# Performance work log

Hardware: AMD Instinct MI355X
Metric: run time of the kernel (lower is better)

Reference implementation:

```python
import jax, jax.numpy as jnp
import numpy as np

NUM_HIDDEN = 256   # per-head dim == model dim in this module
NUM_HEADS = 8
SEQ_LEN = 2048
BATCH = 4
D_K = 256          # self.d_k used for the softmax scale


def setup_inputs() -> dict:
    key = jax.random.key(0)
    ks = jax.random.split(key, 12)
    H, D = NUM_HEADS, NUM_HIDDEN
    init = lambda k, shape: (jax.random.normal(k, shape, dtype=jnp.float32) * 0.02)
    return {
        "query": jax.random.normal(ks[0], (BATCH, SEQ_LEN, D), dtype=jnp.float32),
        "key": jax.random.normal(ks[1], (BATCH, SEQ_LEN, D), dtype=jnp.float32),
        "values": jax.random.normal(ks[2], (BATCH, SEQ_LEN, D), dtype=jnp.float32),
        "Wq": init(ks[3], (H * D, D)), "bq": init(ks[4], (H * D,)),
        "Wk": init(ks[5], (H * D, D)), "bk": init(ks[6], (H * D,)),
        "Wv": init(ks[7], (H * D, D)), "bv": init(ks[8], (H * D,)),
        "Wo": init(ks[9], (D, H * D)), "bo": init(ks[10], (D,)),
    }


def reference(query, key, values, Wq, bq, Wk, bk, Wv, bv, Wo, bo):
    B, S, D = query.shape
    H = Wq.shape[0] // D
    # Linear projections to [B, S, H*D], then the module's raw reshape to [B, H, S, D]
    # (note: this is a plain view, NOT the usual split-heads transpose -> faithful to source)
    q = (jnp.einsum("bsd,ed->bse", query, Wq) + bq).reshape(B, H, S, D)
    k = (jnp.einsum("bsd,ed->bse", key, Wk) + bk).reshape(B, H, S, D)
    v = (jnp.einsum("bsd,ed->bse", values, Wv) + bv).reshape(B, H, S, D)
    # scores: [B, H, S, S], scaled by sqrt(d_k); default path applies no mask
    scores = jnp.einsum("bhqd,bhkd->bhqk", q, k) / jnp.sqrt(jnp.float32(D_K))
    attn = jax.nn.softmax(scores, axis=-1)
    # dropout in eval mode: identity
    out = jnp.einsum("bhqk,bhkd->bhqd", attn, v)            # [B, H, S, D]
    out = out.transpose(0, 2, 1, 3).reshape(B, S, H * D)    # [B, S, H*D]
    return jnp.einsum("bse,de->bsd", out, Wo) + bo          # [B, S, D]
```

## Files before the change

### kernel.cpp

```cpp
#include <hip/hip_runtime.h>
#include <hip/hip_bf16.h>
#include <stdint.h>

#define B_SZ 4
#define H_N 8
#define S_LEN 2048
#define D_HEAD 256
#define HD 2048

typedef __attribute__((ext_vector_type(8))) short bf16x8;
typedef __attribute__((ext_vector_type(4))) float f32x4;
typedef __attribute__((ext_vector_type(4))) uint32_t u32x4;
typedef __hip_bfloat16 bf16;

typedef __attribute__((address_space(1))) const void glob_cv;
typedef __attribute__((address_space(3))) void lds_v;

__device__ __forceinline__ short f2bf(float f) {
  bf16 h = __float2bfloat16(f);
  return *reinterpret_cast<short*>(&h);
}

__device__ __forceinline__ uint32_t cvtpk(float lo, float hi) {
  uint32_t r;
  asm volatile("v_cvt_pk_bf16_f32 %0, %1, %2" : "=v"(r) : "v"(lo), "v"(hi));
  return r;
}

__global__ __launch_bounds__(256) void cvt_all(
    const float* __restrict__ w0, bf16* __restrict__ o0,
    const float* __restrict__ w1, bf16* __restrict__ o1,
    const float* __restrict__ w2, bf16* __restrict__ o2,
    const float* __restrict__ w3, bf16* __restrict__ o3,
    const float* __restrict__ x0, bf16* __restrict__ y0,
    const float* __restrict__ x1, bf16* __restrict__ y1,
    const float* __restrict__ x2, bf16* __restrict__ y2) {
  int bid = blockIdx.x;
  const float* src; bf16* dst; int off;
  if (bid < 1024) {
    int k = bid >> 8; off = (bid & 255) * 2048;
    src = k == 0 ? w0 : k == 1 ? w1 : k == 2 ? w2 : w3;
    dst = k == 0 ? o0 : k == 1 ? o1 : k == 2 ? o2 : o3;
  } else {
    int j = bid - 1024; int k = j >> 10; off = (j & 1023) * 2048;
    src = k == 0 ? x0 : k == 1 ? x1 : x2;
    dst = k == 0 ? y0 : k == 1 ? y1 : y2;
  }
  int i = off + threadIdx.x * 8;
  float4 a = *(const float4*)(src + i);
  float4 b = *(const float4*)(src + i + 4);
  bf16x8 o;
  o[0] = f2bf(a.x); o[1] = f2bf(a.y); o[2] = f2bf(a.z); o[3] = f2bf(a.w);
  o[4] = f2bf(b.x); o[5] = f2bf(b.y); o[6] = f2bf(b.z); o[7] = f2bf(b.w);
  *reinterpret_cast<bf16x8*>(dst + i) = o;
}

__global__ __launch_bounds__(256, 2) void proj3(
    const bf16* __restrict__ A0, const bf16* __restrict__ A1, const bf16* __restrict__ A2,
    const bf16* __restrict__ B0, const bf16* __restrict__ B1, const bf16* __restrict__ B2,
    const float* __restrict__ c0, const float* __restrict__ c1, const float* __restrict__ c2,
    bf16* __restrict__ O0, bf16* __restrict__ O1, bf16* __restrict__ O2) {
  constexpr int HALF = 2 * 128 * 128;
  __shared__ __align__(16) char lds[2 * HALF];

  int which = blockIdx.y;
  const bf16* A = which == 0 ? A0 : which == 1 ? A1 : A2;
  const bf16* Bm = which == 0 ? B0 : which == 1 ? B1 : B2;
  const float* bias = which == 0 ? c0 : which == 1 ? c1 : c2;
  bf16* OutP = which == 0 ? O0 : which == 1 ? O1 : O2;
  float scale = which == 0 ? (1.0f / 16.0f) * 1.44269504f : 1.0f;

  int tid = threadIdx.x;
  int w = tid >> 6, l = tid & 63;
  int l15 = l & 15, lg = l >> 4;
  int wr = w >> 1, wc = w & 1;

  int bid = blockIdx.x;
  int wg = (bid & 7) * 128 + (bid >> 3);
  int mt = wg >> 4, nt = wg & 15;
  int m0 = mt * 128, n0 = nt * 128;

  const size_t K2 = 512;
  char* ldsp = (char*)lds;
  const char* Abase = (const char*)A + (size_t)m0 * K2;
  const char* Bbase = (const char*)Bm + (size_t)n0 * K2;

  auto ISSUE = [&](int buf, int kt) {
    const char* As = Abase + (size_t)kt * 128;
    const char* Bs = Bbase + (size_t)kt * 128;
    char* db = ldsp + buf * HALF;
#pragma unroll
    for (int i = 0; i < 4; ++i) {
      int c = tid + i * 256, row = c >> 3;
      __builtin_amdgcn_global_load_lds((glob_cv*)(As + (size_t)row * K2 + 16 * ((c & 7) ^ (row & 7))),
                                       (lds_v*)(db + c * 16), 16, 0, 0);
    }
#pragma unroll
    for (int i = 0; i < 4; ++i) {
      int c = tid + i * 256, row = c >> 3;
      __builtin_amdgcn_global_load_lds((glob_cv*)(Bs + (size_t)row * K2 + 16 * ((c & 7) ^ (row & 7))),
                                       (lds_v*)(db + 16384 + c * 16), 16, 0, 0);
    }
  };

  f32x4 acc[4][4];
#pragma unroll
  for (int mi = 0; mi < 4; ++mi)
#pragma unroll
    for (int ni = 0; ni < 4; ++ni) acc[mi][ni] = f32x4{0.f, 0.f, 0.f, 0.f};

  ISSUE(0, 0);
  for (int kt = 0; kt < 4; ++kt) {
    int cur = kt & 1;
    if (kt < 3) {
      ISSUE(cur ^ 1, kt + 1);
      asm volatile("s_waitcnt vmcnt(8)" ::: "memory");
    } else {
      asm volatile("s_waitcnt vmcnt(0)" ::: "memory");
    }
    __builtin_amdgcn_s_barrier();
    __builtin_amdgcn_sched_barrier(0);

    const char* bufc = ldsp + cur * HALF;
#pragma unroll
    for (int kb2 = 0; kb2 < 2; ++kb2) {
      int swz = 16 * ((kb2 * 4 + lg) ^ (l15 & 7));
      bf16x8 af[4], bfr[4];
#pragma unroll
      for (int mi = 0; mi < 4; ++mi)
        af[mi] = *(const bf16x8*)(bufc + (wr * 64 + mi * 16 + l15) * 128 + swz);
#pragma unroll
      for (int ni = 0; ni < 4; ++ni)
        bfr[ni] = *(const bf16x8*)(bufc + 16384 + (wc * 64 + ni * 16 + l15) * 128 + swz);
#pragma unroll
      for (int mi = 0; mi < 4; ++mi)
#pragma unroll
        for (int ni = 0; ni < 4; ++ni)
          acc[mi][ni] = __builtin_amdgcn_mfma_f32_16x16x32_bf16(af[mi], bfr[ni], acc[mi][ni], 0, 0, 0);
    }
    __builtin_amdgcn_sched_barrier(0);
    __builtin_amdgcn_s_barrier();
  }

  if (which == 2) {
    bf16* tp = (bf16*)lds;
#pragma unroll
    for (int ni = 0; ni < 4; ++ni) {
      int colL = wc * 64 + ni * 16 + l15;
      float bv = bias[n0 + colL];
#pragma unroll
      for (int mi = 0; mi < 4; ++mi) {
        short4 pk4;
        pk4.x = f2bf(acc[mi][ni][0] + bv);
        pk4.y = f2bf(acc[mi][ni][1] + bv);
        pk4.z = f2bf(acc[mi][ni][2] + bv);
        pk4.w = f2bf(acc[mi][ni][3] + bv);
        *(short4*)(tp + colL * 136 + wr * 64 + mi * 16 + lg * 4) = pk4;
      }
    }
    __syncthreads();
    int b = m0 >> 11, h = (m0 >> 8) & 7;
    int ehi = n0 >> 8, t0 = m0 & 255;
    bf16* vb = OutP + (size_t)(b * 8 + h) * D_HEAD * S_LEN;
#pragma unroll
    for (int p = 0; p < 8; ++p) {
      int colL = p * 16 + (tid >> 4);
      int d = (n0 & 255) + colL;
      int4 v = *(const int4*)(tp + colL * 136 + (tid & 15) * 8);
      *(int4*)(vb + (size_t)d * S_LEN + ehi * 256 + t0 + (tid & 15) * 8) = v;
    }
  } else {
#pragma unroll
    for (int ni = 0; ni < 4; ++ni) {
      int col = n0 + wc * 64 + ni * 16 + l15;
      float bv = bias[col];
#pragma unroll
      for (int mi = 0; mi < 4; ++mi) {
#pragma unroll
        for (int r = 0; r < 4; ++r) {
          float v = (acc[mi][ni][r] + bv) * scale;
          int row = m0 + wr * 64 + mi * 16 + lg * 4 + r;
          int b = row >> 11;
          int h = (row >> 8) & 7;
          int d = col & 255;
          size_t off;
          if (which == 1) {
            int jj = (col >> 8) * 256 + (row & 255);
            off = (((size_t)(b * 8 + h) * S_LEN) + jj) * D_HEAD + d;
          } else {
            int sp = ((row & 255) << 3) | (col >> 8);
            off = (((size_t)(b * 8 + h) * S_LEN) + sp) * D_HEAD + d;
          }
          OutP[off] = __float2bfloat16(v);
        }
      }
    }
  }
}

__global__ __launch_bounds__(256, 2) void out_gemm(const bf16* __restrict__ A,
                                                   const bf16* __restrict__ Bm,
                                                   const float* __restrict__ bias,
                                                   float* __restrict__ Out) {
  constexpr int HALF = 2 * 64 * 128;
  __shared__ __align__(16) char lds[2 * HALF];

  int tid = threadIdx.x;
  int w = tid >> 6, l = tid & 63;
  int l15 = l & 15, lg = l >> 4;
  int wr = w >> 1, wc = w & 1;

  int bid = blockIdx.x;
  int wg = (bid & 7) * 64 + (bid >> 3);
  int mt = wg >> 2, nt = wg & 3;
  int m0 = mt * 64, n0 = nt * 64;

  const size_t K2 = 4096;
  char* ldsp = (char*)lds;
  const char* Abase = (const char*)A + (size_t)m0 * K2;
  const char* Bbase = (const char*)Bm + (size_t)n0 * K2;

  auto ISSUE = [&](int buf, int kt) {
    const char* As = Abase + (size_t)kt * 128;
    const char* Bs = Bbase + (size_t)kt * 128;
    char* db = ldsp + buf * HALF;
#pragma unroll
    for (int i = 0; i < 2; ++i) {
      int c = tid + i * 256, row = c >> 3;
      __builtin_amdgcn_global_load_lds((glob_cv*)(As + (size_t)row * K2 + 16 * ((c & 7) ^ (row & 7))),
                                       (lds_v*)(db + c * 16), 16, 0, 0);
    }
#pragma unroll
    for (int i = 0; i < 2; ++i) {
      int c = tid + i * 256, row = c >> 3;
      __builtin_amdgcn_global_load_lds((glob_cv*)(Bs + (size_t)row * K2 + 16 * ((c & 7) ^ (row & 7))),
                                       (lds_v*)(db + 8192 + c * 16), 16, 0, 0);
    }
  };

  f32x4 acc[2][2];
#pragma unroll
  for (int mi = 0; mi < 2; ++mi)
#pragma unroll
    for (int ni = 0; ni < 2; ++ni) acc[mi][ni] = f32x4{0.f, 0.f, 0.f, 0.f};

  ISSUE(0, 0);
  for (int kt = 0; kt < 32; ++kt) {
    int cur = kt & 1;
    if (kt < 31) {
      ISSUE(cur ^ 1, kt + 1);
      asm volatile("s_waitcnt vmcnt(4)" ::: "memory");
    } else {
      asm volatile("s_waitcnt vmcnt(0)" ::: "memory");
    }
    __builtin_amdgcn_s_barrier();
    __builtin_amdgcn_sched_barrier(0);

    const char* bufc = ldsp + cur * HALF;
#pragma unroll
    for (int kb2 = 0; kb2 < 2; ++kb2) {
      int swz = 16 * ((kb2 * 4 + lg) ^ (l15 & 7));
      bf16x8 af[2], bfr[2];
#pragma unroll
      for (int mi = 0; mi < 2; ++mi)
        af[mi] = *(const bf16x8*)(bufc + (wr * 32 + mi * 16 + l15) * 128 + swz);
#pragma unroll
      for (int ni = 0; ni < 2; ++ni)
        bfr[ni] = *(const bf16x8*)(bufc + 8192 + (wc * 32 + ni * 16 + l15) * 128 + swz);
#pragma unroll
      for (int mi = 0; mi < 2; ++mi)
#pragma unroll
        for (int ni = 0; ni < 2; ++ni)
          acc[mi][ni] = __builtin_amdgcn_mfma_f32_16x16x32_bf16(af[mi], bfr[ni], acc[mi][ni], 0, 0, 0);
    }
    __builtin_amdgcn_sched_barrier(0);
    __builtin_amdgcn_s_barrier();
  }

#pragma unroll
  for (int ni = 0; ni < 2; ++ni) {
    int col = n0 + wc * 32 + ni * 16 + l15;
    float bv = bias[col];
#pragma unroll
    for (int mi = 0; mi < 2; ++mi)
#pragma unroll
      for (int r = 0; r < 4; ++r)
        Out[(size_t)(m0 + wr * 32 + mi * 16 + lg * 4 + r) * 256 + col] = acc[mi][ni][r] + bv;
  }
}

__global__ __launch_bounds__(512, 4) void attn_kernel(const bf16* __restrict__ Qp,
                                                      const bf16* __restrict__ Kp,
                                                      const bf16* __restrict__ Vt,
                                                      bf16* __restrict__ AL) {
  __shared__ __align__(16) bf16 KVs[2 * 16384];

  int tid = threadIdx.x;
  int w = tid >> 6, l = tid & 63;
  int l15 = l & 15, lg = l >> 4;
  int l31 = l & 31, hl = l >> 5;

  int bid = blockIdx.x;
  int xcd = bid & 7, j = bid >> 3;
  int bh = xcd + 8 * (j >> 4);
  int qt = j & 15;

  const bf16* Qb = Qp + (size_t)bh * S_LEN * D_HEAD;
  const bf16* Kb = Kp + (size_t)bh * S_LEN * D_HEAD;
  const bf16* Vb = Vt + (size_t)bh * (size_t)D_HEAD * S_LEN;

  int q0 = qt * 128 + w * 16;

  bf16x8 qf[8];
#pragma unroll
  for (int kb = 0; kb < 8; ++kb)
    qf[kb] = *(const bf16x8*)(Qb + (size_t)(q0 + l15) * D_HEAD + kb * 32 + lg * 8);

  f32x4 acc[16];
#pragma unroll
  for (int n = 0; n < 16; ++n) acc[n] = f32x4{0.f, 0.f, 0.f, 0.f};
  float l_part = 0.f;

  int kvp = 2 * (l31 & 15) + (l31 >> 4);
  const char* pK = (const char*)Kb + (size_t)kvp * 512 + (size_t)(w * 128 + hl * 16);
  const char* pV = (const char*)Vb + (size_t)l * 4096 + (size_t)((w - 4) * 16);
  int dK = w * 4096 + l * 16;
  int dV = 16384 + (w - 4) * 4096 + l * 16;
  char* ldsBase = (char*)&KVs[0];

  auto ISSUE = [&](int buf) {
    char* bb = ldsBase + buf * 32768;
    if (w < 4) {
#pragma unroll
      for (int i = 0; i < 4; ++i)
        __builtin_amdgcn_global_load_lds((glob_cv*)(pK + i * 32),
                                         (lds_v*)(bb + dK + i * 1024), 16, 0, 0);
      pK += 32 * 512;
    } else {
#pragma unroll
      for (int i = 0; i < 4; ++i)
        __builtin_amdgcn_global_load_lds((glob_cv*)(pV + i * 262144),
                                         (lds_v*)(bb + dV + i * 1024), 16, 0, 0);
      pV += 64;
    }
  };

  int krd = lg * 256 + l15 * 8;
  int vrd = 8192 + lg * 2048 + l15 * 8;

  ISSUE(0);

  for (int kt = 0; kt < 64; ++kt) {
    int cur = kt & 1;
    asm volatile("s_waitcnt vmcnt(0)" ::: "memory");
    __builtin_amdgcn_s_barrier();
    __builtin_amdgcn_sched_barrier(0);
    if (kt < 63) ISSUE(cur ^ 1);

    const bf16* bufp = &KVs[cur * 16384];

    f32x4 sc0 = f32x4{0.f, 0.f, 0.f, 0.f}, sc1 = f32x4{0.f, 0.f, 0.f, 0.f};
    __builtin_amdgcn_s_setprio(1);
#pragma unroll
    for (int kb = 0; kb < 8; ++kb) {
      bf16x8 kf0 = *(const bf16x8*)(bufp + krd + kb * 1024);
      bf16x8 kf1 = *(const bf16x8*)(bufp + krd + kb * 1024 + 128);
      sc0 = __builtin_amdgcn_mfma_f32_16x16x32_bf16(kf0, qf[kb], sc0, 0, 0, 0);
      sc1 = __builtin_amdgcn_mfma_f32_16x16x32_bf16(kf1, qf[kb], sc1, 0, 0, 0);
    }
    __builtin_amdgcn_s_setprio(0);

    float p0[4], p1[4];
#pragma unroll
    for (int r = 0; r < 4; ++r) {
      p0[r] = exp2f(sc0[r]);
      p1[r] = exp2f(sc1[r]);
    }
    l_part += (p0[0] + p1[0]) + (p0[1] + p1[1]) + (p0[2] + p1[2]) + (p0[3] + p1[3]);

    union { u32x4 wq; bf16x8 v; } pau;
    pau.wq[0] = cvtpk(p0[0], p1[0]);
    pau.wq[1] = cvtpk(p0[1], p1[1]);
    pau.wq[2] = cvtpk(p0[2], p1[2]);
    pau.wq[3] = cvtpk(p0[3], p1[3]);
    bf16x8 pa = pau.v;

    __builtin_amdgcn_s_setprio(1);
#pragma unroll
    for (int n = 0; n < 16; ++n) {
      bf16x8 vbf = *(const bf16x8*)(bufp + vrd + n * 128);
      acc[n] = __builtin_amdgcn_mfma_f32_16x16x32_bf16(pa, vbf, acc[n], 0, 0, 0);
    }
    __builtin_amdgcn_s_setprio(0);
  }

  float ts = l_part;
  ts += __shfl_xor(ts, 16);
  ts += __shfl_xor(ts, 32);
  float invl = 1.0f / ts;
  float i0 = __shfl(invl, lg * 4 + 0);
  float i1 = __shfl(invl, lg * 4 + 1);
  float i2 = __shfl(invl, lg * 4 + 2);
  float i3 = __shfl(invl, lg * 4 + 3);
  int b = bh >> 3, h = bh & 7;
#pragma unroll
  for (int r = 0; r < 4; ++r) {
    float inv = r == 0 ? i0 : r == 1 ? i1 : r == 2 ? i2 : i3;
    int q = q0 + lg * 4 + r;
    bf16* orow = AL + ((size_t)b * S_LEN + q) * HD + h * D_HEAD;
#pragma unroll
    for (int n = 0; n < 16; ++n)
      orow[n * 16 + l15] = __float2bfloat16(acc[n][r] * inv);
  }
}

extern "C" void kernel_launch(void* const* d_in, const int* in_sizes, int n_in,
                              void* d_out, int out_size, void* d_ws, size_t ws_size,
                              hipStream_t stream) {
  (void)in_sizes; (void)n_in; (void)out_size; (void)ws_size;
  const float* query  = (const float*)d_in[0];
  const float* key    = (const float*)d_in[1];
  const float* values = (const float*)d_in[2];
  const float* Wq = (const float*)d_in[3];
  const float* bq = (const float*)d_in[4];
  const float* Wk = (const float*)d_in[5];
  const float* bk = (const float*)d_in[6];
  const float* Wv = (const float*)d_in[7];
  const float* bv = (const float*)d_in[8];
  const float* Wo = (const float*)d_in[9];
  const float* bo = (const float*)d_in[10];
  float* out = (float*)d_out;

  bf16* ws = (bf16*)d_ws;
  const size_t NP = (size_t)B_SZ * H_N * S_LEN * D_HEAD;
  const size_t NW = (size_t)HD * D_HEAD;
  const size_t NX = (size_t)B_SZ * S_LEN * D_HEAD;
  bf16* Qp  = ws;
  bf16* Kp  = Qp + NP;
  bf16* Vtp = Kp + NP;
  bf16* ALb = Vtp + NP;
  bf16* Wqb = ALb + NP;
  bf16* Wkb = Wqb + NW;
  bf16* Wvb = Wkb + NW;
  bf16* Wob = Wvb + NW;
  bf16* Xqb = ALb;
  bf16* Xkb = ALb + NX;
  bf16* Xvb = ALb + 2 * NX;

  cvt_all<<<4096, 256, 0, stream>>>(Wq, Wqb, Wk, Wkb, Wv, Wvb, Wo, Wob,
                                    query, Xqb, key, Xkb, values, Xvb);

  proj3<<<dim3(1024, 3), 256, 0, stream>>>(Xqb, Xkb, Xvb, Wqb, Wkb, Wvb,
                                           bq, bk, bv, Qp, Kp, Vtp);

  attn_kernel<<<512, 512, 0, stream>>>(Qp, Kp, Vtp, ALb);

  out_gemm<<<512, 256, 0, stream>>>(ALb, Wob, bo, out);
}
```

Measured before the change: 239.0 us.

## Give each attention wave two 16-row query tiles and halve block threads

Each wave of the attention kernel now handles 32 query rows as two 16-row tiles, so every K and V fragment read from LDS feeds two MFMAs instead of one. The block drops from 8 waves to 4, and each wave issues twice as many global-to-LDS loads to fill the same K/V tile. This is meant to cut LDS read traffic per MFMA. In exchange it doubles the accumulator and Q-fragment registers per wave and lowers the launch-bounds occupancy target, which could limit latency hiding.

```diff
diff --git a/kernel.cpp b/kernel.cpp
--- a/kernel.cpp
+++ b/kernel.cpp
@@ -289,7 +289,7 @@
   }
 }
 
-__global__ __launch_bounds__(512, 4) void attn_kernel(const bf16* __restrict__ Qp,
+__global__ __launch_bounds__(256, 2) void attn_kernel(const bf16* __restrict__ Qp,
                                                       const bf16* __restrict__ Kp,
                                                       const bf16* __restrict__ Vt,
                                                       bf16* __restrict__ AL) {
@@ -309,38 +309,43 @@
   const bf16* Kb = Kp + (size_t)bh * S_LEN * D_HEAD;
   const bf16* Vb = Vt + (size_t)bh * (size_t)D_HEAD * S_LEN;
 
-  int q0 = qt * 128 + w * 16;
-
-  bf16x8 qf[8];
-#pragma unroll
-  for (int kb = 0; kb < 8; ++kb)
-    qf[kb] = *(const bf16x8*)(Qb + (size_t)(q0 + l15) * D_HEAD + kb * 32 + lg * 8);
-
-  f32x4 acc[16];
-#pragma unroll
-  for (int n = 0; n < 16; ++n) acc[n] = f32x4{0.f, 0.f, 0.f, 0.f};
-  float l_part = 0.f;
+  int q0 = qt * 128 + w * 32;
+
+  bf16x8 qf0[8], qf1[8];
+#pragma unroll
+  for (int kb = 0; kb < 8; ++kb) {
+    qf0[kb] = *(const bf16x8*)(Qb + (size_t)(q0 + l15) * D_HEAD + kb * 32 + lg * 8);
+    qf1[kb] = *(const bf16x8*)(Qb + (size_t)(q0 + 16 + l15) * D_HEAD + kb * 32 + lg * 8);
+  }
+
+  f32x4 acc0[16], acc1[16];
+#pragma unroll
+  for (int n = 0; n < 16; ++n) {
+    acc0[n] = f32x4{0.f, 0.f, 0.f, 0.f};
+    acc1[n] = f32x4{0.f, 0.f, 0.f, 0.f};
+  }
+  float lp0 = 0.f, lp1 = 0.f;
 
   int kvp = 2 * (l31 & 15) + (l31 >> 4);
-  const char* pK = (const char*)Kb + (size_t)kvp * 512 + (size_t)(w * 128 + hl * 16);
-  const char* pV = (const char*)Vb + (size_t)l * 4096 + (size_t)((w - 4) * 16);
-  int dK = w * 4096 + l * 16;
-  int dV = 16384 + (w - 4) * 4096 + l * 16;
+  const char* pK = (const char*)Kb + (size_t)kvp * 512 + (size_t)(w * 256 + hl * 16);
+  const char* pV = (const char*)Vb + (size_t)l * 4096 + (size_t)((w - 2) * 32);
+  int dK = w * 8192 + l * 16;
+  int dV = 16384 + (w - 2) * 8192 + l * 16;
   char* ldsBase = (char*)&KVs[0];
 
   auto ISSUE = [&](int buf) {
     char* bb = ldsBase + buf * 32768;
-    if (w < 4) {
-#pragma unroll
-      for (int i = 0; i < 4; ++i)
+    if (w < 2) {
+#pragma unroll
+      for (int i = 0; i < 8; ++i)
         __builtin_amdgcn_global_load_lds((glob_cv*)(pK + i * 32),
                                          (lds_v*)(bb + dK + i * 1024), 16, 0, 0);
       pK += 32 * 512;
     } else {
 #pragma unroll
-      for (int i = 0; i < 4; ++i)
-        __builtin_amdgcn_global_load_lds((glob_cv*)(pV + i * 262144),
-                                         (lds_v*)(bb + dV + i * 1024), 16, 0, 0);
+      for (int i = 0; i < 8; ++i)
+        __builtin_amdgcn_global_load_lds((glob_cv*)(pV + (i & 3) * 262144 + (i >> 2) * 16),
+                                         (lds_v*)(bb + dV + (i & 3) * 1024 + (i >> 2) * 4096), 16, 0, 0);
       pV += 64;
     }
   };
@@ -359,58 +364,72 @@
 
     const bf16* bufp = &KVs[cur * 16384];
 
-    f32x4 sc0 = f32x4{0.f, 0.f, 0.f, 0.f}, sc1 = f32x4{0.f, 0.f, 0.f, 0.f};
+    f32x4 s00 = f32x4{0.f,0.f,0.f,0.f}, s01 = f32x4{0.f,0.f,0.f,0.f};
+    f32x4 s10 = f32x4{0.f,0.f,0.f,0.f}, s11 = f32x4{0.f,0.f,0.f,0.f};
     __builtin_amdgcn_s_setprio(1);
 #pragma unroll
     for (int kb = 0; kb < 8; ++kb) {
       bf16x8 kf0 = *(const bf16x8*)(bufp + krd + kb * 1024);
       bf16x8 kf1 = *(const bf16x8*)(bufp + krd + kb * 1024 + 128);
-      sc0 = __builtin_amdgcn_mfma_f32_16x16x32_bf16(kf0, qf[kb], sc0, 0, 0, 0);
-      sc1 = __builtin_amdgcn_mfma_f32_16x16x32_bf16(kf1, qf[kb], sc1, 0, 0, 0);
+      s00 = __builtin_amdgcn_mfma_f32_16x16x32_bf16(kf0, qf0[kb], s00, 0, 0, 0);
+      s01 = __builtin_amdgcn_mfma_f32_16x16x32_bf16(kf1, qf0[kb], s01, 0, 0, 0);
+      s10 = __builtin_amdgcn_mfma_f32_16x16x32_bf16(kf0, qf1[kb], s10, 0, 0, 0);
+      s11 = __builtin_amdgcn_mfma_f32_16x16x32_bf16(kf1, qf1[kb], s11, 0, 0, 0);
     }
     __builtin_amdgcn_s_setprio(0);
 
-    float p0[4], p1[4];
+    float p00[4], p01[4], p10[4], p11[4];
 #pragma unroll
     for (int r = 0; r < 4; ++r) {
-      p0[r] = exp2f(sc0[r]);
-      p1[r] = exp2f(sc1[r]);
-    }
-    l_part += (p0[0] + p1[0]) + (p0[1] + p1[1]) + (p0[2] + p1[2]) + (p0[3] + p1[3]);
-
-    union { u32x4 wq; bf16x8 v; } pau;
-    pau.wq[0] = cvtpk(p0[0], p1[0]);
-    pau.wq[1] = cvtpk(p0[1], p1[1]);
-    pau.wq[2] = cvtpk(p0[2], p1[2]);
-    pau.wq[3] = cvtpk(p0[3], p1[3]);
-    bf16x8 pa = pau.v;
+      p00[r] = exp2f(s00[r]); p01[r] = exp2f(s01[r]);
+      p10[r] = exp2f(s10[r]); p11[r] = exp2f(s11[r]);
+    }
+    lp0 += (p00[0] + p01[0]) + (p00[1] + p01[1]) + (p00[2] + p01[2]) + (p00[3] + p01[3]);
+    lp1 += (p10[0] + p11[0]) + (p10[1] + p11[1]) + (p10[2] + p11[2]) + (p10[3] + p11[3]);
+
+    union { u32x4 wq; bf16x8 v; } pu0, pu1;
+    pu0.wq[0] = cvtpk(p00[0], p01[0]); pu0.wq[1] = cvtpk(p00[1], p01[1]);
+    pu0.wq[2] = cvtpk(p00[2], p01[2]); pu0.wq[3] = cvtpk(p00[3], p01[3]);
+    pu1.wq[0] = cvtpk(p10[0], p11[0]); pu1.wq[1] = cvtpk(p10[1], p11[1]);
+    pu1.wq[2] = cvtpk(p10[2], p11[2]); pu1.wq[3] = cvtpk(p10[3], p11[3]);
+    bf16x8 pa0 = pu0.v, pa1 = pu1.v;
 
     __builtin_amdgcn_s_setprio(1);
 #pragma unroll
     for (int n = 0; n < 16; ++n) {
       bf16x8 vbf = *(const bf16x8*)(bufp + vrd + n * 128);
-      acc[n] = __builtin_amdgcn_mfma_f32_16x16x32_bf16(pa, vbf, acc[n], 0, 0, 0);
+      acc0[n] = __builtin_amdgcn_mfma_f32_16x16x32_bf16(pa0, vbf, acc0[n], 0, 0, 0);
+      acc1[n] = __builtin_amdgcn_mfma_f32_16x16x32_bf16(pa1, vbf, acc1[n], 0, 0, 0);
     }
     __builtin_amdgcn_s_setprio(0);
   }
 
-  float ts = l_part;
-  ts += __shfl_xor(ts, 16);
-  ts += __shfl_xor(ts, 32);
-  float invl = 1.0f / ts;
-  float i0 = __shfl(invl, lg * 4 + 0);
-  float i1 = __shfl(invl, lg * 4 + 1);
-  float i2 = __shfl(invl, lg * 4 + 2);
-  float i3 = __shfl(invl, lg * 4 + 3);
+  float t0 = lp0;
+  t0 += __shfl_xor(t0, 16);
+  t0 += __shfl_xor(t0, 32);
+  float inv0 = 1.0f / t0;
+  float t1 = lp1;
+  t1 += __shfl_xor(t1, 16);
+  t1 += __shfl_xor(t1, 32);
+  float inv1 = 1.0f / t1;
+  float i00 = __shfl(inv0, lg * 4 + 0), i01 = __shfl(inv0, lg * 4 + 1);
+  float i02 = __shfl(inv0, lg * 4 + 2), i03 = __shfl(inv0, lg * 4 + 3);
+  float i10 = __shfl(inv1, lg * 4 + 0), i11 = __shfl(inv1, lg * 4 + 1);
+  float i12 = __shfl(inv1, lg * 4 + 2), i13 = __shfl(inv1, lg * 4 + 3);
   int b = bh >> 3, h = bh & 7;
 #pragma unroll
   for (int r = 0; r < 4; ++r) {
-    float inv = r == 0 ? i0 : r == 1 ? i1 : r == 2 ? i2 : i3;
-    int q = q0 + lg * 4 + r;
-    bf16* orow = AL + ((size_t)b * S_LEN + q) * HD + h * D_HEAD;
-#pragma unroll
-    for (int n = 0; n < 16; ++n)
-      orow[n * 16 + l15] = __float2bfloat16(acc[n][r] * inv);
+    float v0 = r == 0 ? i00 : r == 1 ? i01 : r == 2 ? i02 : i03;
+    float v1 = r == 0 ? i10 : r == 1 ? i11 : r == 2 ? i12 : i13;
+    int qa = q0 + lg * 4 + r;
+    int qb = qa + 16;
+    bf16* orow0 = AL + ((size_t)b * S_LEN + qa) * HD + h * D_HEAD;
+    bf16* orow1 = AL + ((size_t)b * S_LEN + qb) * HD + h * D_HEAD;
+#pragma unroll
+    for (int n = 0; n < 16; ++n) {
+      orow0[n * 16 + l15] = __float2bfloat16(acc0[n][r] * v0);
+      orow1[n * 16 + l15] = __float2bfloat16(acc1[n][r] * v1);
+    }
   }
 }
 
@@ -453,7 +472,7 @@
   proj3<<<dim3(1024, 3), 256, 0, stream>>>(Xqb, Xkb, Xvb, Wqb, Wkb, Wvb,
                                            bq, bk, bv, Qp, Kp, Vtp);
 
-  attn_kernel<<<512, 512, 0, stream>>>(Qp, Kp, Vtp, ALb);
+  attn_kernel<<<512, 256, 0, stream>>>(Qp, Kp, Vtp, ALb);
 
   out_gemm<<<512, 256, 0, stream>>>(ALb, Wob, bo, out);
 }
```

Result: faster. 233.1 us, median of 2 (-2.5%).
